# Kernel tuning notes

Hardware: AMD Instinct MI355X
Metric: run time of the kernel (lower is better)

Reference implementation:

```python
import jax, jax.numpy as jnp
import numpy as np
from jax import lax

NL, HID, DIN, DST, DCONV, DTR = 4, 256, 512, 16, 4, 16  # layers, d_model, expand*d_model, d_state, d_conv, dt_rank
B, H, W = 4, 256, 256


def setup_inputs() -> dict:
    key = jax.random.key(0)
    ks = jax.random.split(key, 8)
    def n(k, s, sc=0.02):
        return jax.random.normal(k, s, dtype=jnp.float32) * sc
    return {
        "x": jax.random.normal(ks[0], (B, 3, H, W), dtype=jnp.float32),
        "conv1_w": n(ks[1], (HID // 2, 3, 3, 3), 0.1), "conv1_b": jnp.zeros((HID // 2,), jnp.float32),
        "gn1_w": jnp.ones((HID // 2,), jnp.float32), "gn1_b": jnp.zeros((HID // 2,), jnp.float32),
        "conv2_w": n(ks[2], (HID, HID // 2, 3, 3), 0.05), "conv2_b": jnp.zeros((HID,), jnp.float32),
        "gn2_w": jnp.ones((HID,), jnp.float32), "gn2_b": jnp.zeros((HID,), jnp.float32),
        "ln_w": jnp.ones((NL, HID), jnp.float32), "ln_b": jnp.zeros((NL, HID), jnp.float32),
        "in_proj_w": n(ks[3], (NL, 2 * DIN, HID)),
        "conv1d_w": n(ks[4], (NL, DIN, 1, DCONV), 0.1), "conv1d_b": jnp.zeros((NL, DIN), jnp.float32),
        "x_proj_w": n(ks[5], (NL, DTR + 2 * DST, DIN)),
        "dt_proj_w": n(ks[6], (NL, DIN, DTR), 0.1),
        "dt_proj_b": jnp.full((NL, DIN), -4.6, dtype=jnp.float32),  # softplus(-4.6) ~ 0.01
        "A_log": jnp.broadcast_to(jnp.log(jnp.arange(1, DST + 1, dtype=jnp.float32)), (NL, DIN, DST)) + jnp.zeros((NL, DIN, DST), jnp.float32),
        "D": jnp.ones((NL, DIN), jnp.float32),
        "out_proj_w": n(ks[7], (NL, HID, DIN)),
    }


def conv2d_s2(x, w, b):
    y = lax.conv_general_dilated(x, w, (2, 2), [(1, 1), (1, 1)],
                                 dimension_numbers=('NCHW', 'OIHW', 'NCHW'))
    return y + b[None, :, None, None]


def group_norm(x, w, b, groups=8, eps=1e-5):
    Bb, C, Hh, Ww = x.shape
    xg = x.reshape(Bb, groups, C // groups, Hh, Ww)
    m = xg.mean((2, 3, 4), keepdims=True)
    v = xg.var((2, 3, 4), keepdims=True)
    xg = (xg - m) * lax.rsqrt(v + eps)
    return xg.reshape(Bb, C, Hh, Ww) * w[None, :, None, None] + b[None, :, None, None]


def layer_norm(x, w, b, eps=1e-5):
    m = x.mean(-1, keepdims=True)
    v = x.var(-1, keepdims=True)
    return (x - m) * lax.rsqrt(v + eps) * w + b


def mamba(x, ipw, cw, cb, xpw, dpw, dpb, A_log, Dp, opw):
    # x: [B, L, HID]
    Bb, L, _ = x.shape
    xz = jnp.einsum('bld,ed->ble', x, ipw)           # [B, L, 2*DIN]
    xc, z = jnp.split(xz, 2, axis=-1)
    # depthwise causal conv1d over L
    u = xc.transpose(0, 2, 1)                        # [B, DIN, L]
    u = lax.conv_general_dilated(u, cw, (1,), [(DCONV - 1, 0)],
                                 dimension_numbers=('NCH', 'OIH', 'NCH'),
                                 feature_group_count=DIN)
    xc = jax.nn.silu(u + cb[None, :, None]).transpose(0, 2, 1)  # [B, L, DIN]
    x_dbl = jnp.einsum('bld,ed->ble', xc, xpw)       # [B, L, DTR+2*DST]
    dt, Bm, Cm = jnp.split(x_dbl, [DTR, DTR + DST], axis=-1)
    delta = jax.nn.softplus(jnp.einsum('blr,dr->bld', dt, dpw) + dpb)  # [B, L, DIN]
    A = -jnp.exp(A_log)                              # [DIN, DST]
    dA = jnp.exp(jnp.einsum('bld,dn->bldn', delta, A))
    dBu = jnp.einsum('bld,bln,bld->bldn', delta, Bm, xc)

    def step(h, inp):
        dA_t, dBu_t, C_t = inp
        h = dA_t * h + dBu_t                         # [B, DIN, DST]
        return h, jnp.einsum('bdn,bn->bd', h, C_t)

    h0 = jnp.zeros((Bb, DIN, DST), x.dtype)
    _, ys = lax.scan(step, h0, (dA.transpose(1, 0, 2, 3), dBu.transpose(1, 0, 2, 3), Cm.transpose(1, 0, 2)))
    y = ys.transpose(1, 0, 2) + xc * Dp              # [B, L, DIN]
    y = y * jax.nn.silu(z)
    return jnp.einsum('bld,ed->ble', y, opw)         # [B, L, HID]


def reference(x, conv1_w, conv1_b, gn1_w, gn1_b, conv2_w, conv2_b, gn2_w, gn2_b,
              ln_w, ln_b, in_proj_w, conv1d_w, conv1d_b, x_proj_w, dt_proj_w,
              dt_proj_b, A_log, D, out_proj_w):
    y = jax.nn.silu(group_norm(conv2d_s2(x, conv1_w, conv1_b), gn1_w, gn1_b))
    y = jax.nn.silu(group_norm(conv2d_s2(y, conv2_w, conv2_b), gn2_w, gn2_b))
    Bb, C, h, w = y.shape
    s = y.reshape(Bb, C, h * w).transpose(0, 2, 1)   # b (h w) c
    for i in range(NL):
        s = s + mamba(layer_norm(s, ln_w[i], ln_b[i]), in_proj_w[i], conv1d_w[i],
                      conv1d_b[i], x_proj_w[i], dt_proj_w[i], dt_proj_b[i],
                      A_log[i], D[i], out_proj_w[i])
    return (s, h, w)
```

## Files before the change

### kernel.cpp

```cpp
#include <hip/hip_runtime.h>
#include <math.h>

#define BB 4
#define C1 128
#define H1 128
#define W1 128
#define C2 256
#define H2 64
#define W2 64
#define LSEQ 4096
#define HID 256
#define DIN 512
#define DST 16
#define DTR 16
#define NL 4
#define NCHUNK 128
#define LCH 32

typedef unsigned short u16;
using short8 = __attribute__((ext_vector_type(8))) short;
using f32x4  = __attribute__((ext_vector_type(4))) float;
using f32x2  = __attribute__((ext_vector_type(2))) float;

static __device__ __forceinline__ float dsilu(float x){
    return x / (1.0f + __expf(-x));
}
static __device__ __forceinline__ u16 f2bf(float f){
    unsigned u = __float_as_uint(f);
    u += 0x7FFF + ((u >> 16) & 1);
    return (u16)(u >> 16);
}
static __device__ __forceinline__ float bf2f(u16 v){
    return __uint_as_float(((unsigned)v) << 16);
}

#define GLL16(g, l) __builtin_amdgcn_global_load_lds( \
    (const __attribute__((address_space(1))) void*)(g), \
    (__attribute__((address_space(3))) void*)(l), 16, 0, 0)

__global__ void f2bf_kernel(const float* __restrict__ src, u16* __restrict__ dst){
    int idx = blockIdx.x * 256 + threadIdx.x;
    dst[idx] = f2bf(src[idx]);
}
__global__ void wdt_prep_kernel(const float* __restrict__ xpw, const float* __restrict__ dpw,
                                u16* __restrict__ wcomb){
    int idx = blockIdx.x * 256 + threadIdx.x;
    int k = idx & 511;
    int n = (idx >> 9) % 640;
    int layer = idx / (640*512);
    u16 val = 0;
    if(n < 512){
        const float* dp = dpw + ((long)layer*512 + n)*16;
        const float* xp = xpw + (long)layer*48*512 + k;
        float acc = 0.f;
        #pragma unroll
        for(int r = 0; r < 16; ++r) acc = fmaf(dp[r], xp[(long)r*512], acc);
        val = f2bf(acc);
    } else if(n < 544){
        int row = n - 512 + 16;
        val = f2bf(xpw[((long)layer*48 + row)*512 + k]);
    }
    wcomb[((long)layer*640 + n)*512 + k] = val;
}
__global__ void c2w_prep_kernel(const float* __restrict__ src, u16* __restrict__ dst){
    int idx = blockIdx.x * 256 + threadIdx.x;
    int ci = idx & 127, p = (idx >> 7) % 9, co = idx / (9*128);
    int kh = p / 3, kw = p - 3*kh;
    dst[idx] = f2bf(src[((co*128 + ci)*3 + kh)*3 + kw]);
}
__global__ void xt_zero_kernel(unsigned* __restrict__ xt){
    xt[blockIdx.x * 256 + threadIdx.x] = 0;
}

__global__ __launch_bounds__(256) void conv1_kernel(
        const float* __restrict__ x, const float* __restrict__ w,
        const float* __restrict__ bias, float* __restrict__ y){
    __shared__ float xs[9][260];
    int oh = blockIdx.x, b = blockIdx.y;
    int tid = threadIdx.x;
    #pragma unroll
    for(int r = 0; r < 9; ++r){
        int ci = r / 3, kh = r - 3*ci;
        int ih = 2*oh - 1 + kh;
        float v = 0.f;
        if(ih >= 0) v = x[((b*3 + ci)*256 + ih)*256 + tid];
        xs[r][tid + 1] = v;
        if(tid == 0) xs[r][0] = 0.f;
    }
    __syncthreads();
    int co = tid >> 1, h = tid & 1;
    float wr[27];
    #pragma unroll
    for(int j = 0; j < 27; ++j) wr[j] = w[co*27 + j];
    float bz = bias[co];
    long obase = ((long)((b*128 + co)*128 + oh))*128 + h*64;
    #pragma unroll 4
    for(int i = 0; i < 64; ++i){
        int iw0 = 2*(h*64 + i);
        float acc = bz;
        #pragma unroll
        for(int r = 0; r < 9; ++r){
            acc = fmaf(xs[r][iw0+0], wr[r*3+0], acc);
            acc = fmaf(xs[r][iw0+1], wr[r*3+1], acc);
            acc = fmaf(xs[r][iw0+2], wr[r*3+2], acc);
        }
        y[obase + i] = acc;
    }
}

__global__ void zero_stats_kernel(float* __restrict__ stats){
    stats[threadIdx.x] = 0.0f;
}

__global__ void gn_stats_kernel(const float* __restrict__ x, float* __restrict__ stats,
                                int elems_per_group){
    const int EPB = 16384;
    long base = (long)blockIdx.x * EPB;
    int g = (int)(base / elems_per_group);
    float s = 0.f, ss = 0.f;
    for(int j = threadIdx.x; j < EPB; j += 256){
        float v = x[base + j];
        s += v; ss += v*v;
    }
    #pragma unroll
    for(int off = 32; off; off >>= 1){
        s  += __shfl_down(s,  off);
        ss += __shfl_down(ss, off);
    }
    __shared__ float ls[4], lss[4];
    int wid = threadIdx.x >> 6, lane = threadIdx.x & 63;
    if(lane == 0){ ls[wid] = s; lss[wid] = ss; }
    __syncthreads();
    if(threadIdx.x == 0){
        atomicAdd(&stats[g],      ls[0]+ls[1]+ls[2]+ls[3]);
        atomicAdd(&stats[32+g], lss[0]+lss[1]+lss[2]+lss[3]);
    }
}

__global__ void gn1_transform_kernel(const float* __restrict__ y1, const float* __restrict__ stats,
                                     const float* __restrict__ w, const float* __restrict__ bias,
                                     u16* __restrict__ xt){
    __shared__ float tile[32][33];
    int b = blockIdx.z >> 7, ih = blockIdx.z & 127;
    int c0 = blockIdx.y * 32, w0 = blockIdx.x * 32;
    int tx = threadIdx.x, ty = threadIdx.y;
    const float cnt = 16.f * 128.f * 128.f;
    #pragma unroll
    for(int i = 0; i < 4; ++i){
        int ci = c0 + ty + i*8;
        int g = b*8 + (ci >> 4);
        float mean = stats[g] / cnt;
        float var  = stats[32+g] / cnt - mean*mean;
        float rstd = rsqrtf(var + 1e-5f);
        float v = y1[(((long)(b*C1 + ci))*H1 + ih)*W1 + w0 + tx];
        tile[ty + i*8][tx] = dsilu((v - mean) * rstd * w[ci] + bias[ci]);
    }
    __syncthreads();
    #pragma unroll
    for(int i = 0; i < 4; ++i){
        int iwl = ty + i*8;
        xt[((long)(b*130 + ih + 1)*130 + (w0 + iwl + 1))*128 + c0 + tx] = f2bf(tile[tx][iwl]);
    }
}

__global__ __launch_bounds__(256) void conv2gemm_bf16_kernel(
        const u16* __restrict__ xt, const u16* __restrict__ w2,
        const float* __restrict__ bias, float* __restrict__ y2t){
    __shared__ u16 Asm[128*32];
    __shared__ u16 Bsm[128*32];
    int m0 = blockIdx.x * 128, n0 = blockIdx.y * 128;
    int tid = threadIdx.x;
    long abase[2]; const u16* bbase[2];
    #pragma unroll
    for(int it = 0; it < 2; ++it){
        int c = it*256 + tid;
        int r = c >> 2, q = (c & 3) * 8;
        int m = m0 + r;
        int b = m >> 12, oh = (m >> 6) & 63, ow = m & 63;
        abase[it] = ((long)(b*130 + 2*oh)*130 + 2*ow)*128 + q;
        bbase[it] = w2 + (long)(n0 + r)*1152 + q;
    }
    int wave = tid >> 6, lane = tid & 63;
    int wr = wave >> 1, wc = wave & 1;
    int lm = lane & 15, lq = lane >> 4;
    f32x4 acc[4][4] = {};
    #pragma unroll 1
    for(int p = 0; p < 9; ++p){
        int kh = p / 3, kw = p - 3*kh;
        int aoff = (kh*130 + kw)*128;
        #pragma unroll 1
        for(int ci0 = 0; ci0 < 128; ci0 += 32){
            #pragma unroll
            for(int it = 0; it < 2; ++it){
                int c = it*256 + tid;
                GLL16(xt + abase[it] + aoff + ci0, &Asm[c*8]);
                GLL16(bbase[it] + p*128 + ci0, &Bsm[c*8]);
            }
            __syncthreads();
            short8 af[4], bf[4];
            #pragma unroll
            for(int i = 0; i < 4; ++i){
                af[i] = *(const short8*)&Asm[(wr*64 + i*16 + lm)*32 + lq*8];
                bf[i] = *(const short8*)&Bsm[(wc*64 + i*16 + lm)*32 + lq*8];
            }
            #pragma unroll
            for(int i = 0; i < 4; ++i)
                #pragma unroll
                for(int j = 0; j < 4; ++j)
                    acc[i][j] = __builtin_amdgcn_mfma_f32_16x16x32_bf16(af[i], bf[j], acc[i][j], 0, 0, 0);
            __syncthreads();
        }
    }
    #pragma unroll
    for(int i = 0; i < 4; ++i){
        long row = m0 + wr*64 + i*16 + lq*4;
        #pragma unroll
        for(int j = 0; j < 4; ++j){
            int col = n0 + wc*64 + j*16 + lm;
            float bz = bias[col];
            #pragma unroll
            for(int r = 0; r < 4; ++r)
                y2t[(row + r)*256L + col] = acc[i][j][r] + bz;
        }
    }
}

__global__ void gn2t_stats_kernel(const float* __restrict__ y2t, float* __restrict__ stats){
    int b = blockIdx.y;
    long row0 = (long)b*LSEQ + blockIdx.x*64;
    int c = threadIdx.x;
    float s = 0.f, ss = 0.f;
    for(int r = 0; r < 64; ++r){
        float v = y2t[(row0 + r)*C2 + c];
        s += v; ss += v*v;
    }
    #pragma unroll
    for(int off = 16; off; off >>= 1){
        s  += __shfl_down(s,  off);
        ss += __shfl_down(ss, off);
    }
    if((c & 31) == 0){
        int g = b*8 + (c >> 5);
        atomicAdd(&stats[g], s);
        atomicAdd(&stats[32+g], ss);
    }
}

__global__ void gn2t_apply_ln_kernel(const float* __restrict__ y2t, const float* __restrict__ stats,
                                     const float* __restrict__ gw, const float* __restrict__ gb,
                                     const float* __restrict__ lw, const float* __restrict__ lb,
                                     float* __restrict__ s, u16* __restrict__ xln){
    long row = blockIdx.x;
    int c = threadIdx.x;
    int b = (int)(row >> 12);
    int g = b*8 + (c >> 5);
    const float cnt = 32.f * (float)LSEQ;
    float mean = stats[g] / cnt;
    float var  = stats[32+g] / cnt - mean*mean;
    float rstd = rsqrtf(var + 1e-5f);
    float v = dsilu((y2t[row*HID + c] - mean) * rstd * gw[c] + gb[c]);
    s[row*HID + c] = v;
    float sm = v, sq = v*v;
    #pragma unroll
    for(int off = 32; off; off >>= 1){
        sm += __shfl_down(sm, off);
        sq += __shfl_down(sq, off);
    }
    __shared__ float pa[4], pb[4], res[2];
    int wid = c >> 6, lane = c & 63;
    if(lane == 0){ pa[wid] = sm; pb[wid] = sq; }
    __syncthreads();
    if(c == 0){
        float t  = pa[0]+pa[1]+pa[2]+pa[3];
        float tt = pb[0]+pb[1]+pb[2]+pb[3];
        float m2 = t / 256.f;
        float v2 = tt / 256.f - m2*m2;
        res[0] = m2; res[1] = rsqrtf(v2 + 1e-5f);
    }
    __syncthreads();
    xln[row*HID + c] = f2bf((v - res[0]) * res[1] * lw[c] + lb[c]);
}

__global__ __launch_bounds__(256) void gemm_bf16_kernel(
        const u16* __restrict__ A, const u16* __restrict__ B, void* __restrict__ Cv,
        int K, int Nact, int ldc, int mode){
    __shared__ u16 Asm[128*32];
    __shared__ u16 Bsm[128*32];
    int m0 = blockIdx.x * 128, n0 = blockIdx.y * 128;
    int tid = threadIdx.x;
    int wave = tid >> 6, lane = tid & 63;
    int wr = wave >> 1, wc = wave & 1;
    int lm = lane & 15, lq = lane >> 4;
    f32x4 acc[4][4] = {};
    for(int k0 = 0; k0 < K; k0 += 32){
        #pragma unroll
        for(int it = 0; it < 2; ++it){
            int c = it*256 + tid;
            int row = c >> 2, kq = (c & 3) * 8;
            GLL16(A + (long)(m0 + row)*K + k0 + kq, &Asm[c*8]);
            GLL16(B + (long)(n0 + row)*K + k0 + kq, &Bsm[c*8]);
        }
        __syncthreads();
        short8 af[4], bf[4];
        #pragma unroll
        for(int i = 0; i < 4; ++i){
            af[i] = *(const short8*)&Asm[(wr*64 + i*16 + lm)*32 + lq*8];
            bf[i] = *(const short8*)&Bsm[(wc*64 + i*16 + lm)*32 + lq*8];
        }
        #pragma unroll
        for(int i = 0; i < 4; ++i)
            #pragma unroll
            for(int j = 0; j < 4; ++j)
                acc[i][j] = __builtin_amdgcn_mfma_f32_16x16x32_bf16(af[i], bf[j], acc[i][j], 0, 0, 0);
        __syncthreads();
    }
    #pragma unroll
    for(int i = 0; i < 4; ++i){
        long row = m0 + wr*64 + i*16 + lq*4;
        #pragma unroll
        for(int j = 0; j < 4; ++j){
            int col = n0 + wc*64 + j*16 + lm;
            if(col < Nact){
                #pragma unroll
                for(int r = 0; r < 4; ++r){
                    long idx = (row + r)*(long)ldc + col;
                    if(mode == 2) ((u16*)Cv)[idx] = f2bf(acc[i][j][r]);
                    else          ((float*)Cv)[idx] = acc[i][j][r];
                }
            }
        }
    }
}

__global__ __launch_bounds__(256) void gemm_dtbc_kernel(
        const u16* __restrict__ A, const u16* __restrict__ B,
        const float* __restrict__ dpb, u16* __restrict__ dv,
        float* __restrict__ xdbl32){
    __shared__ u16 Asm[128*32];
    __shared__ u16 Bsm[128*32];
    int m0 = blockIdx.x * 128, n0 = blockIdx.y * 128;
    int tid = threadIdx.x;
    int wave = tid >> 6, lane = tid & 63;
    int wr = wave >> 1, wc = wave & 1;
    int lm = lane & 15, lq = lane >> 4;
    f32x4 acc[4][4] = {};
    for(int k0 = 0; k0 < 512; k0 += 32){
        #pragma unroll
        for(int it = 0; it < 2; ++it){
            int c = it*256 + tid;
            int row = c >> 2, kq = (c & 3) * 8;
            GLL16(A + (long)(m0 + row)*512 + k0 + kq, &Asm[c*8]);
            GLL16(B + (long)(n0 + row)*512 + k0 + kq, &Bsm[c*8]);
        }
        __syncthreads();
        short8 af[4], bf[4];
        #pragma unroll
        for(int i = 0; i < 4; ++i){
            af[i] = *(const short8*)&Asm[(wr*64 + i*16 + lm)*32 + lq*8];
            bf[i] = *(const short8*)&Bsm[(wc*64 + i*16 + lm)*32 + lq*8];
        }
        #pragma unroll
        for(int i = 0; i < 4; ++i)
            #pragma unroll
            for(int j = 0; j < 4; ++j)
                acc[i][j] = __builtin_amdgcn_mfma_f32_16x16x32_bf16(af[i], bf[j], acc[i][j], 0, 0, 0);
        __syncthreads();
    }
    if(n0 < 512){
        #pragma unroll
        for(int i = 0; i < 4; ++i){
            long row = m0 + wr*64 + i*16 + lq*4;
            #pragma unroll
            for(int j = 0; j < 4; ++j){
                int col = n0 + wc*64 + j*16 + lm;
                float bz = dpb[col];
                #pragma unroll
                for(int r = 0; r < 4; ++r){
                    float v = acc[i][j][r] + bz;
                    v = (v > 20.f) ? v : __logf(1.f + __expf(v));
                    dv[(row + r)*512L + col] = f2bf(v);
                }
            }
        }
    } else {
        #pragma unroll
        for(int i = 0; i < 4; ++i){
            long row = m0 + wr*64 + i*16 + lq*4;
            #pragma unroll
            for(int j = 0; j < 4; ++j){
                int lcol = wc*64 + j*16 + lm;
                if(lcol < 32){
                    #pragma unroll
                    for(int r = 0; r < 4; ++r)
                        xdbl32[(row + r)*32L + lcol] = acc[i][j][r];
                }
            }
        }
    }
}

__global__ __launch_bounds__(256) void gemm_out_ln_kernel(
        const u16* __restrict__ A, const u16* __restrict__ B,
        float* __restrict__ s, u16* __restrict__ xln,
        const float* __restrict__ lw, const float* __restrict__ lb){
    __shared__ u16 Asm[64*32];
    __shared__ u16 Bsm[256*32];
    int m0 = blockIdx.x * 64;
    int tid = threadIdx.x;
    int w = tid >> 6, lane = tid & 63;
    int lm = lane & 15, lq = lane >> 4;
    f32x4 acc[16] = {};
    for(int k0 = 0; k0 < 512; k0 += 32){
        {
            int row = tid >> 2, kq = (tid & 3) * 8;
            GLL16(A + (long)(m0 + row)*512 + k0 + kq, &Asm[tid*8]);
        }
        #pragma unroll
        for(int it = 0; it < 4; ++it){
            int c = it*256 + tid;
            int row = c >> 2, kq = (c & 3) * 8;
            GLL16(B + (long)row*512 + k0 + kq, &Bsm[c*8]);
        }
        __syncthreads();
        short8 af = *(const short8*)&Asm[(w*16 + lm)*32 + lq*8];
        #pragma unroll
        for(int j = 0; j < 16; ++j){
            short8 bf = *(const short8*)&Bsm[(j*16 + lm)*32 + lq*8];
            acc[j] = __builtin_amdgcn_mfma_f32_16x16x32_bf16(af, bf, acc[j], 0, 0, 0);
        }
        __syncthreads();
    }
    int row0 = m0 + w*16 + lq*4;
    float psum[4] = {0.f,0.f,0.f,0.f}, psq[4] = {0.f,0.f,0.f,0.f};
    #pragma unroll
    for(int j = 0; j < 16; ++j){
        int col = j*16 + lm;
        #pragma unroll
        for(int r = 0; r < 4; ++r){
            long idx = (long)(row0 + r)*HID + col;
            float v = s[idx] + acc[j][r];
            acc[j][r] = v;
            s[idx] = v;
            psum[r] += v; psq[r] += v*v;
        }
    }
    #pragma unroll
    for(int mask = 1; mask <= 8; mask <<= 1){
        #pragma unroll
        for(int r = 0; r < 4; ++r){
            psum[r] += __shfl_xor(psum[r], mask);
            psq[r]  += __shfl_xor(psq[r],  mask);
        }
    }
    float mean[4], rstd[4];
    #pragma unroll
    for(int r = 0; r < 4; ++r){
        mean[r] = psum[r] * (1.f/256.f);
        float var = psq[r] * (1.f/256.f) - mean[r]*mean[r];
        rstd[r] = rsqrtf(var + 1e-5f);
    }
    #pragma unroll
    for(int j = 0; j < 16; ++j){
        int col = j*16 + lm;
        float wv = lw[col], bv = lb[col];
        #pragma unroll
        for(int r = 0; r < 4; ++r){
            long idx = (long)(row0 + r)*HID + col;
            xln[idx] = f2bf((acc[j][r] - mean[r]) * rstd[r] * wv + bv);
        }
    }
}

__global__ void conv1d_silu_kernel(const u16* __restrict__ xz, const float* __restrict__ w,
                                   const float* __restrict__ bias, u16* __restrict__ xcv){
    int idx = blockIdx.x * 256 + threadIdx.x;
    int e = idx * 8;
    int d0 = e & 511;
    long m = e >> 9;
    int l = (int)(m & 4095);
    short8 xrow[4];
    const u16* xp = xz + m*(2*DIN) + d0;
    #pragma unroll
    for(int j = 0; j < 4; ++j){
        int t = l - 3 + j;
        if(t >= 0) xrow[j] = *(const short8*)(xp + (long)(j-3)*(2*DIN));
        else       xrow[j] = (short8){0,0,0,0,0,0,0,0};
    }
    float wv[8][4];
    #pragma unroll
    for(int k = 0; k < 8; k += 2){
        float4 a = *(const float4*)(w + (d0+k)*4);
        float4 b = *(const float4*)(w + (d0+k+1)*4);
        wv[k][0]=a.x; wv[k][1]=a.y; wv[k][2]=a.z; wv[k][3]=a.w;
        wv[k+1][0]=b.x; wv[k+1][1]=b.y; wv[k+1][2]=b.z; wv[k+1][3]=b.w;
    }
    float bz[8];
    {
        float4 a = *(const float4*)(bias + d0);
        float4 b = *(const float4*)(bias + d0 + 4);
        bz[0]=a.x; bz[1]=a.y; bz[2]=a.z; bz[3]=a.w;
        bz[4]=b.x; bz[5]=b.y; bz[6]=b.z; bz[7]=b.w;
    }
    short8 out;
    #pragma unroll
    for(int k = 0; k < 8; ++k){
        float acc = bz[k];
        #pragma unroll
        for(int j = 0; j < 4; ++j)
            acc = fmaf(bf2f((u16)xrow[j][k]), wv[k][j], acc);
        out[k] = (short)f2bf(dsilu(acc));
    }
    *(short8*)(xcv + m*DIN + d0) = out;
}

__global__ __launch_bounds__(256) void scan1_kernel(
        const u16* __restrict__ xcvb, const u16* __restrict__ dvin,
        const float* __restrict__ xdbl32, const float* __restrict__ Alog,
        float* __restrict__ aprod, float* __restrict__ hend){
    int d = blockIdx.y * 256 + threadIdx.x;
    int c = blockIdx.x;
    int b = blockIdx.z;
    __shared__ float bm[LCH][16];
    {
        int t = threadIdx.x >> 4, n = threadIdx.x & 15;
        #pragma unroll
        for(int it = 0; it < 2; ++it){
            long p = ((long)(b*LSEQ + c*LCH + t + it*16))*32;
            bm[t + it*16][n] = xdbl32[p + n];
        }
    }
    __syncthreads();
    float An[16];
    #pragma unroll
    for(int n = 0; n < 16; ++n)
        An[n] = -__expf(Alog[d*16 + n]);
    float An0 = An[0];
    bool structural = true;
    #pragma unroll
    for(int n = 0; n < 16; ++n)
        structural = structural && (fabsf(An[n] - (float)(n+1)*An0) <= 1e-3f*(float)(n+1));
    long base = ((long)(b*LSEQ + c*LCH))*DIN + d;
    long ob = (((long)(b*NCHUNK + c))*DIN + d)*16;
    if(structural){
        f32x2 h2[8];
        #pragma unroll
        for(int i = 0; i < 8; ++i) h2[i] = (f32x2){0.f, 0.f};
        float sumdv = 0.f;
        float xv_n = bf2f(xcvb[base]);
        float dv_n = bf2f(dvin[base]);
        for(int t = 0; t < LCH; ++t){
            float xv = xv_n, dv = dv_n;
            if(t + 1 < LCH){
                xv_n = bf2f(xcvb[base + (long)(t+1)*DIN]);
                dv_n = bf2f(dvin[base + (long)(t+1)*DIN]);
            }
            sumdv += dv;
            float db = dv * xv;
            float r1 = __expf(dv * An0);
            float r2 = r1 * r1;
            f32x2 rr = {r2, r2};
            f32x2 e2[8];
            e2[0] = (f32x2){r1, r2};
            #pragma unroll
            for(int i = 1; i < 8; ++i) e2[i] = e2[i-1] * rr;
            f32x2 db2 = {db, db};
            const f32x2* b2 = (const f32x2*)&bm[t][0];
            #pragma unroll
            for(int i = 0; i < 8; ++i) h2[i] = e2[i]*h2[i] + db2*b2[i];
        }
        float R = __expf(An0 * sumdv);
        float Rp = R;
        const float* hp = (const float*)h2;
        #pragma unroll
        for(int n = 0; n < 16; ++n){
            aprod[ob+n] = Rp; Rp *= R;
            hend[ob+n] = hp[n];
        }
    } else {
        float h[16], ap[16];
        #pragma unroll
        for(int n = 0; n < 16; ++n){ h[n] = 0.f; ap[n] = 1.f; }
        for(int t = 0; t < LCH; ++t){
            float dv = bf2f(dvin[base + (long)t*DIN]);
            float db = dv * bf2f(xcvb[base + (long)t*DIN]);
            #pragma unroll
            for(int n = 0; n < 16; ++n){
                float e = __expf(dv * An[n]);
                ap[n] *= e;
                h[n] = fmaf(e, h[n], db * bm[t][n]);
            }
        }
        #pragma unroll
        for(int n = 0; n < 16; ++n){ aprod[ob+n] = ap[n]; hend[ob+n] = h[n]; }
    }
}

__global__ void scan2_kernel(const float* __restrict__ aprod, const float* __restrict__ hend,
                             float* __restrict__ hinit){
    int idx = blockIdx.x * 256 + threadIdx.x;
    int n = idx & 15, d = (idx >> 4) & 511, b = idx >> 13;
    const long stride = (long)DIN * 16;
    long p0 = (((long)(b*NCHUNK))*DIN + d)*16 + n;
    float h = 0.f;
    for(int c = 0; c < NCHUNK; c += 8){
        float a[8], e[8];
        #pragma unroll
        for(int j = 0; j < 8; ++j){
            long p = p0 + (long)(c + j)*stride;
            a[j] = aprod[p]; e[j] = hend[p];
        }
        #pragma unroll
        for(int j = 0; j < 8; ++j){
            hinit[p0 + (long)(c + j)*stride] = h;
            h = fmaf(a[j], h, e[j]);
        }
    }
}

__global__ __launch_bounds__(256) void scan3_kernel(
        const u16* __restrict__ xcvb, const u16* __restrict__ dvin,
        const float* __restrict__ xdbl32, const float* __restrict__ Alog,
        const float* __restrict__ hinit, const float* __restrict__ Dp,
        const u16* __restrict__ xz, u16* __restrict__ yout){
    int d = blockIdx.y * 256 + threadIdx.x;
    int c = blockIdx.x;
    int b = blockIdx.z;
    __shared__ float bm[LCH][16], cm[LCH][16];
    {
        int t = threadIdx.x >> 4, n = threadIdx.x & 15;
        #pragma unroll
        for(int it = 0; it < 2; ++it){
            long p = ((long)(b*LSEQ + c*LCH + t + it*16))*32;
            bm[t + it*16][n] = xdbl32[p + n];
            cm[t + it*16][n] = xdbl32[p + 16 + n];
        }
    }
    __syncthreads();
    float An[16];
    long hb = (((long)(b*NCHUNK + c))*DIN + d)*16;
    #pragma unroll
    for(int n = 0; n < 16; ++n)
        An[n] = -__expf(Alog[d*16 + n]);
    float An0 = An[0];
    bool structural = true;
    #pragma unroll
    for(int n = 0; n < 16; ++n)
        structural = structural && (fabsf(An[n] - (float)(n+1)*An0) <= 1e-3f*(float)(n+1));
    float Dv = Dp[d];
    long base  = ((long)(b*LSEQ + c*LCH))*DIN + d;
    long zbase = ((long)(b*LSEQ + c*LCH))*(2*DIN) + DIN + d;
    if(structural){
        f32x2 h2[8];
        {
            const f32x2* hi = (const f32x2*)&hinit[hb];
            #pragma unroll
            for(int i = 0; i < 8; ++i) h2[i] = hi[i];
        }
        float xv_n = bf2f(xcvb[base]);
        float z_n  = bf2f(xz[zbase]);
        float dv_n = bf2f(dvin[base]);
        for(int t = 0; t < LCH; ++t){
            float xv = xv_n, z = z_n, dv = dv_n;
            if(t + 1 < LCH){
                xv_n = bf2f(xcvb[base + (long)(t+1)*DIN]);
                z_n  = bf2f(xz[zbase + (long)(t+1)*(2*DIN)]);
                dv_n = bf2f(dvin[base + (long)(t+1)*DIN]);
            }
            float db = dv * xv;
            float r1 = __expf(dv * An0);
            float r2 = r1 * r1;
            f32x2 rr = {r2, r2};
            f32x2 e2[8];
            e2[0] = (f32x2){r1, r2};
            #pragma unroll
            for(int i = 1; i < 8; ++i) e2[i] = e2[i-1] * rr;
            f32x2 db2 = {db, db};
            const f32x2* b2 = (const f32x2*)&bm[t][0];
            const f32x2* c2 = (const f32x2*)&cm[t][0];
            f32x2 y2 = {0.f, 0.f};
            #pragma unroll
            for(int i = 0; i < 8; ++i){
                h2[i] = e2[i]*h2[i] + db2*b2[i];
                y2 = y2 + h2[i]*c2[i];
            }
            float y = y2[0] + y2[1];
            y = fmaf(xv, Dv, y);
            yout[base + (long)t*DIN] = f2bf(y * dsilu(z));
        }
    } else {
        float h[16];
        #pragma unroll
        for(int n = 0; n < 16; ++n) h[n] = hinit[hb + n];
        for(int t = 0; t < LCH; ++t){
            float dv = bf2f(dvin[base + (long)t*DIN]);
            float xv = bf2f(xcvb[base + (long)t*DIN]);
            float db = dv * xv;
            float y = 0.f;
            #pragma unroll
            for(int n = 0; n < 16; ++n){
                float e = __expf(dv * An[n]);
                h[n] = fmaf(e, h[n], db * bm[t][n]);
                y = fmaf(h[n], cm[t][n], y);
            }
            y = fmaf(xv, Dv, y);
            float z = bf2f(xz[zbase + (long)t*(2*DIN)]);
            yout[base + (long)t*DIN] = f2bf(y * dsilu(z));
        }
    }
}

__global__ void copyout_kernel(const float* __restrict__ s, float* __restrict__ out, int out_size){
    int idx = blockIdx.x * 256 + threadIdx.x;
    if(idx >= out_size) return;
    out[idx] = (idx < BB*LSEQ*HID) ? s[idx] : 64.0f;
}

extern "C" void kernel_launch(void* const* d_in, const int* in_sizes, int n_in,
                              void* d_out, int out_size, void* d_ws, size_t ws_size,
                              hipStream_t stream){
    const float* x        = (const float*)d_in[0];
    const float* conv1_w  = (const float*)d_in[1];
    const float* conv1_b  = (const float*)d_in[2];
    const float* gn1_w    = (const float*)d_in[3];
    const float* gn1_b    = (const float*)d_in[4];
    const float* conv2_w  = (const float*)d_in[5];
    const float* conv2_b  = (const float*)d_in[6];
    const float* gn2_w    = (const float*)d_in[7];
    const float* gn2_b    = (const float*)d_in[8];
    const float* ln_w     = (const float*)d_in[9];
    const float* ln_b     = (const float*)d_in[10];
    const float* in_proj  = (const float*)d_in[11];
    const float* c1d_w    = (const float*)d_in[12];
    const float* c1d_b    = (const float*)d_in[13];
    const float* x_proj   = (const float*)d_in[14];
    const float* dt_w     = (const float*)d_in[15];
    const float* dt_b     = (const float*)d_in[16];
    const float* A_log    = (const float*)d_in[17];
    const float* Dvec     = (const float*)d_in[18];
    const float* out_proj = (const float*)d_in[19];

    float* ws = (float*)d_ws;
    float* s      = ws;
    u16*   xz_bf  = (u16*)(ws + 4194304);
    float* y1     = ws + 4194304;
    u16*   xt     = (u16*)(ws + 12582912);
    u16*   xcv_bf = (u16*)(ws + 16909312);
    float* y2t    = ws + 16909312;
    u16*   xln_bf = (u16*)(ws + 21103616);
    float* xdbl   = ws + 23200768;
    float* aprod  = ws + 23987200;
    float* hendb  = ws + 28181504;
    u16*   y_bf   = (u16*)aprod;
    float* hinit  = ws + 32375808;
    float* stats  = ws + 36570112;
    u16*   ipw_bf = (u16*)(ws + 36570176);
    u16*   opw_bf = ipw_bf + 1048576;
    u16*   c2w_bf = opw_bf + 524288;
    u16*   dv_bf  = (u16*)(ws + 37635200);
    u16*   wcomb  = (u16*)(ws + 41829504);

    f2bf_kernel<<<4096, 256, 0, stream>>>(in_proj, ipw_bf);
    f2bf_kernel<<<2048, 256, 0, stream>>>(out_proj, opw_bf);
    c2w_prep_kernel<<<1152, 256, 0, stream>>>(conv2_w, c2w_bf);
    wdt_prep_kernel<<<5120, 256, 0, stream>>>(x_proj, dt_w, wcomb);

    conv1_kernel<<<dim3(128,4), 256, 0, stream>>>(x, conv1_w, conv1_b, y1);
    zero_stats_kernel<<<1, 64, 0, stream>>>(stats);
    gn_stats_kernel<<<512, 256, 0, stream>>>(y1, stats, 16*H1*W1);
    xt_zero_kernel<<<16900, 256, 0, stream>>>((unsigned*)xt);
    gn1_transform_kernel<<<dim3(4,4,512), dim3(32,8), 0, stream>>>(y1, stats, gn1_w, gn1_b, xt);
    conv2gemm_bf16_kernel<<<dim3(128,2), 256, 0, stream>>>(xt, c2w_bf, conv2_b, y2t);
    zero_stats_kernel<<<1, 64, 0, stream>>>(stats);
    gn2t_stats_kernel<<<dim3(64,4), 256, 0, stream>>>(y2t, stats);
    gn2t_apply_ln_kernel<<<16384, 256, 0, stream>>>(y2t, stats, gn2_w, gn2_b,
                                                    ln_w, ln_b, s, xln_bf);

    for(int layer = 0; layer < NL; ++layer){
        const float* cw  = c1d_w + (long)layer*DIN*4;
        const float* cb  = c1d_b + (long)layer*DIN;
        const float* dpb = dt_b  + (long)layer*DIN;
        const float* Al  = A_log + (long)layer*DIN*DST;
        const float* Dl  = Dvec  + (long)layer*DIN;
        int lnext = (layer + 1) & 3;

        gemm_bf16_kernel<<<dim3(128,8), 256, 0, stream>>>(
            xln_bf, ipw_bf + (long)layer*1024*256, xz_bf, HID, 2*DIN, 2*DIN, 2);
        conv1d_silu_kernel<<<4096, 256, 0, stream>>>(xz_bf, cw, cb, xcv_bf);
        gemm_dtbc_kernel<<<dim3(128,5), 256, 0, stream>>>(
            xcv_bf, wcomb + (long)layer*640*512, dpb, dv_bf, xdbl);
        scan1_kernel<<<dim3(NCHUNK,2,BB), 256, 0, stream>>>(
            xcv_bf, dv_bf, xdbl, Al, aprod, hendb);
        scan2_kernel<<<128, 256, 0, stream>>>(aprod, hendb, hinit);
        scan3_kernel<<<dim3(NCHUNK,2,BB), 256, 0, stream>>>(
            xcv_bf, dv_bf, xdbl, Al, hinit, Dl, xz_bf, y_bf);
        gemm_out_ln_kernel<<<256, 256, 0, stream>>>(
            y_bf, opw_bf + (long)layer*256*512, s, xln_bf,
            ln_w + lnext*HID, ln_b + lnext*HID);
    }

    copyout_kernel<<<(out_size + 255)/256, 256, 0, stream>>>(s, (float*)d_out, out_size);
}
```

Baseline: 865.6 us.

## Fuse GroupNorm statistics into conv epilogues and shorten scan power chain

GroupNorm sum and sum-of-squares accumulation moves into the conv1 and conv2 GEMM epilogues, so the separate stats kernels that re-read y1 and y2t are removed. The scan kernels build the decay powers with a log-depth ladder instead of a serial multiply chain, and read B/C as 4-wide vectors. The workspace layout is compacted, with dv_bf reusing the xt buffer. The epilogue reductions add shuffles and atomics, and the power ladder can change float rounding slightly.

```diff
diff --git a/kernel.cpp b/kernel.cpp
--- a/kernel.cpp
+++ b/kernel.cpp
@@ -74,7 +74,8 @@
 
 __global__ __launch_bounds__(256) void conv1_kernel(
         const float* __restrict__ x, const float* __restrict__ w,
-        const float* __restrict__ bias, float* __restrict__ y){
+        const float* __restrict__ bias, float* __restrict__ y,
+        float* __restrict__ stats){
     __shared__ float xs[9][260];
     int oh = blockIdx.x, b = blockIdx.y;
     int tid = threadIdx.x;
@@ -94,6 +95,7 @@
     for(int j = 0; j < 27; ++j) wr[j] = w[co*27 + j];
     float bz = bias[co];
     long obase = ((long)((b*128 + co)*128 + oh))*128 + h*64;
+    float s1 = 0.f, s2 = 0.f;
     #pragma unroll 4
     for(int i = 0; i < 64; ++i){
         int iw0 = 2*(h*64 + i);
@@ -105,36 +107,22 @@
             acc = fmaf(xs[r][iw0+2], wr[r*3+2], acc);
         }
         y[obase + i] = acc;
+        s1 += acc; s2 += acc*acc;
+    }
+    #pragma unroll
+    for(int mask = 16; mask; mask >>= 1){
+        s1 += __shfl_xor(s1, mask);
+        s2 += __shfl_xor(s2, mask);
+    }
+    if((tid & 31) == 0){
+        int g = b*8 + (tid >> 5);
+        atomicAdd(&stats[g], s1);
+        atomicAdd(&stats[32+g], s2);
     }
 }
 
 __global__ void zero_stats_kernel(float* __restrict__ stats){
     stats[threadIdx.x] = 0.0f;
-}
-
-__global__ void gn_stats_kernel(const float* __restrict__ x, float* __restrict__ stats,
-                                int elems_per_group){
-    const int EPB = 16384;
-    long base = (long)blockIdx.x * EPB;
-    int g = (int)(base / elems_per_group);
-    float s = 0.f, ss = 0.f;
-    for(int j = threadIdx.x; j < EPB; j += 256){
-        float v = x[base + j];
-        s += v; ss += v*v;
-    }
-    #pragma unroll
-    for(int off = 32; off; off >>= 1){
-        s  += __shfl_down(s,  off);
-        ss += __shfl_down(ss, off);
-    }
-    __shared__ float ls[4], lss[4];
-    int wid = threadIdx.x >> 6, lane = threadIdx.x & 63;
-    if(lane == 0){ ls[wid] = s; lss[wid] = ss; }
-    __syncthreads();
-    if(threadIdx.x == 0){
-        atomicAdd(&stats[g],      ls[0]+ls[1]+ls[2]+ls[3]);
-        atomicAdd(&stats[32+g], lss[0]+lss[1]+lss[2]+lss[3]);
-    }
 }
 
 __global__ void gn1_transform_kernel(const float* __restrict__ y1, const float* __restrict__ stats,
@@ -165,7 +153,8 @@
 
 __global__ __launch_bounds__(256) void conv2gemm_bf16_kernel(
         const u16* __restrict__ xt, const u16* __restrict__ w2,
-        const float* __restrict__ bias, float* __restrict__ y2t){
+        const float* __restrict__ bias, float* __restrict__ y2t,
+        float* __restrict__ stats){
     __shared__ u16 Asm[128*32];
     __shared__ u16 Bsm[128*32];
     int m0 = blockIdx.x * 128, n0 = blockIdx.y * 128;
@@ -211,6 +200,7 @@
             __syncthreads();
         }
     }
+    float gs[2] = {0.f, 0.f}, gq[2] = {0.f, 0.f};
     #pragma unroll
     for(int i = 0; i < 4; ++i){
         long row = m0 + wr*64 + i*16 + lq*4;
@@ -218,31 +208,31 @@
         for(int j = 0; j < 4; ++j){
             int col = n0 + wc*64 + j*16 + lm;
             float bz = bias[col];
-            #pragma unroll
-            for(int r = 0; r < 4; ++r)
-                y2t[(row + r)*256L + col] = acc[i][j][r] + bz;
-        }
-    }
-}
-
-__global__ void gn2t_stats_kernel(const float* __restrict__ y2t, float* __restrict__ stats){
-    int b = blockIdx.y;
-    long row0 = (long)b*LSEQ + blockIdx.x*64;
-    int c = threadIdx.x;
-    float s = 0.f, ss = 0.f;
-    for(int r = 0; r < 64; ++r){
-        float v = y2t[(row0 + r)*C2 + c];
-        s += v; ss += v*v;
-    }
-    #pragma unroll
-    for(int off = 16; off; off >>= 1){
-        s  += __shfl_down(s,  off);
-        ss += __shfl_down(ss, off);
-    }
-    if((c & 31) == 0){
-        int g = b*8 + (c >> 5);
-        atomicAdd(&stats[g], s);
-        atomicAdd(&stats[32+g], ss);
+            int lg = j >> 1;
+            #pragma unroll
+            for(int r = 0; r < 4; ++r){
+                float v = acc[i][j][r] + bz;
+                y2t[(row + r)*256L + col] = v;
+                gs[lg] += v; gq[lg] += v*v;
+            }
+        }
+    }
+    #pragma unroll
+    for(int mask = 32; mask; mask >>= 1){
+        #pragma unroll
+        for(int l = 0; l < 2; ++l){
+            gs[l] += __shfl_xor(gs[l], mask);
+            gq[l] += __shfl_xor(gq[l], mask);
+        }
+    }
+    if(lane == 0){
+        int b = blockIdx.x >> 5;
+        int gbase = b*8 + (n0 >> 5) + wc*2;
+        #pragma unroll
+        for(int l = 0; l < 2; ++l){
+            atomicAdd(&stats[gbase + l], gs[l]);
+            atomicAdd(&stats[32 + gbase + l], gq[l]);
+        }
     }
 }
 
@@ -513,6 +503,19 @@
     *(short8*)(xcv + m*DIN + d0) = out;
 }
 
+static __device__ __forceinline__ void pow_ladder(float r1, f32x2* e2){
+    float r2 = r1*r1, r4 = r2*r2, r8 = r4*r4;
+    f32x2 v2 = {r2, r2}, v4 = {r4, r4}, v8 = {r8, r8};
+    e2[0] = (f32x2){r1, r2};
+    e2[1] = e2[0] * v2;
+    e2[2] = e2[0] * v4;
+    e2[3] = e2[1] * v4;
+    e2[4] = e2[0] * v8;
+    e2[5] = e2[1] * v8;
+    e2[6] = e2[2] * v8;
+    e2[7] = e2[3] * v8;
+}
+
 __global__ __launch_bounds__(256) void scan1_kernel(
         const u16* __restrict__ xcvb, const u16* __restrict__ dvin,
         const float* __restrict__ xdbl32, const float* __restrict__ Alog,
@@ -557,16 +560,17 @@
             sumdv += dv;
             float db = dv * xv;
             float r1 = __expf(dv * An0);
-            float r2 = r1 * r1;
-            f32x2 rr = {r2, r2};
             f32x2 e2[8];
-            e2[0] = (f32x2){r1, r2};
-            #pragma unroll
-            for(int i = 1; i < 8; ++i) e2[i] = e2[i-1] * rr;
+            pow_ladder(r1, e2);
             f32x2 db2 = {db, db};
-            const f32x2* b2 = (const f32x2*)&bm[t][0];
-            #pragma unroll
-            for(int i = 0; i < 8; ++i) h2[i] = e2[i]*h2[i] + db2*b2[i];
+            const f32x4* b4 = (const f32x4*)&bm[t][0];
+            #pragma unroll
+            for(int q = 0; q < 4; ++q){
+                f32x4 bq = b4[q];
+                f32x2 p0 = {bq[0], bq[1]}, p1 = {bq[2], bq[3]};
+                h2[2*q]   = e2[2*q]  *h2[2*q]   + db2*p0;
+                h2[2*q+1] = e2[2*q+1]*h2[2*q+1] + db2*p1;
+            }
         }
         float R = __expf(An0 * sumdv);
         float Rp = R;
@@ -668,20 +672,21 @@
             }
             float db = dv * xv;
             float r1 = __expf(dv * An0);
-            float r2 = r1 * r1;
-            f32x2 rr = {r2, r2};
             f32x2 e2[8];
-            e2[0] = (f32x2){r1, r2};
-            #pragma unroll
-            for(int i = 1; i < 8; ++i) e2[i] = e2[i-1] * rr;
+            pow_ladder(r1, e2);
             f32x2 db2 = {db, db};
-            const f32x2* b2 = (const f32x2*)&bm[t][0];
-            const f32x2* c2 = (const f32x2*)&cm[t][0];
+            const f32x4* b4 = (const f32x4*)&bm[t][0];
+            const f32x4* c4 = (const f32x4*)&cm[t][0];
             f32x2 y2 = {0.f, 0.f};
             #pragma unroll
-            for(int i = 0; i < 8; ++i){
-                h2[i] = e2[i]*h2[i] + db2*b2[i];
-                y2 = y2 + h2[i]*c2[i];
+            for(int q = 0; q < 4; ++q){
+                f32x4 bq = b4[q], cq = c4[q];
+                f32x2 pb0 = {bq[0], bq[1]}, pb1 = {bq[2], bq[3]};
+                f32x2 pc0 = {cq[0], cq[1]}, pc1 = {cq[2], cq[3]};
+                h2[2*q]   = e2[2*q]  *h2[2*q]   + db2*pb0;
+                h2[2*q+1] = e2[2*q+1]*h2[2*q+1] + db2*pb1;
+                y2 = y2 + h2[2*q]*pc0;
+                y2 = y2 + h2[2*q+1]*pc1;
             }
             float y = y2[0] + y2[1];
             y = fmaf(xv, Dv, y);
@@ -744,34 +749,32 @@
     u16*   xz_bf  = (u16*)(ws + 4194304);
     float* y1     = ws + 4194304;
     u16*   xt     = (u16*)(ws + 12582912);
+    u16*   dv_bf  = xt;
     u16*   xcv_bf = (u16*)(ws + 16909312);
     float* y2t    = ws + 16909312;
     u16*   xln_bf = (u16*)(ws + 21103616);
     float* xdbl   = ws + 23200768;
-    float* aprod  = ws + 23987200;
-    float* hendb  = ws + 28181504;
+    float* aprod  = ws + 23725056;
+    float* hendb  = ws + 27919360;
     u16*   y_bf   = (u16*)aprod;
-    float* hinit  = ws + 32375808;
-    float* stats  = ws + 36570112;
-    u16*   ipw_bf = (u16*)(ws + 36570176);
+    float* hinit  = ws + 32113664;
+    float* stats  = ws + 36307968;
+    u16*   ipw_bf = (u16*)(ws + 36308032);
     u16*   opw_bf = ipw_bf + 1048576;
     u16*   c2w_bf = opw_bf + 524288;
-    u16*   dv_bf  = (u16*)(ws + 37635200);
-    u16*   wcomb  = (u16*)(ws + 41829504);
+    u16*   wcomb  = (u16*)(ws + 37241920);
 
     f2bf_kernel<<<4096, 256, 0, stream>>>(in_proj, ipw_bf);
     f2bf_kernel<<<2048, 256, 0, stream>>>(out_proj, opw_bf);
     c2w_prep_kernel<<<1152, 256, 0, stream>>>(conv2_w, c2w_bf);
     wdt_prep_kernel<<<5120, 256, 0, stream>>>(x_proj, dt_w, wcomb);
 
-    conv1_kernel<<<dim3(128,4), 256, 0, stream>>>(x, conv1_w, conv1_b, y1);
     zero_stats_kernel<<<1, 64, 0, stream>>>(stats);
-    gn_stats_kernel<<<512, 256, 0, stream>>>(y1, stats, 16*H1*W1);
+    conv1_kernel<<<dim3(128,4), 256, 0, stream>>>(x, conv1_w, conv1_b, y1, stats);
     xt_zero_kernel<<<16900, 256, 0, stream>>>((unsigned*)xt);
     gn1_transform_kernel<<<dim3(4,4,512), dim3(32,8), 0, stream>>>(y1, stats, gn1_w, gn1_b, xt);
-    conv2gemm_bf16_kernel<<<dim3(128,2), 256, 0, stream>>>(xt, c2w_bf, conv2_b, y2t);
     zero_stats_kernel<<<1, 64, 0, stream>>>(stats);
-    gn2t_stats_kernel<<<dim3(64,4), 256, 0, stream>>>(y2t, stats);
+    conv2gemm_bf16_kernel<<<dim3(128,2), 256, 0, stream>>>(xt, c2w_bf, conv2_b, y2t, stats);
     gn2t_apply_ln_kernel<<<16384, 256, 0, stream>>>(y2t, stats, gn2_w, gn2_b,
                                                     ln_w, ln_b, s, xln_bf);
 
```

After: 866.6 us. Within noise of the previous version (+0.1%).
